# Performance work log

Measured on AMD Instinct MI355X. Metric: run time of the kernel, lower is better.

Reference implementation:

```python
import jax, jax.numpy as jnp
import numpy as np

NUM_HEADS = 12


def setup_inputs() -> dict:
    key = jax.random.key(0)
    k0, k1, k2 = jax.random.split(key, 3)
    B, S, D = 2, 2048, 1536
    scale = 1.0 / np.sqrt(D)
    return {
        "hidden_states": jax.random.normal(k0, (B, S, D), dtype=jnp.float32),
        "W_fc": jax.random.normal(k1, (D, D), dtype=jnp.float32) * scale,
        "b_fc": jnp.zeros((D,), dtype=jnp.float32),
        "W_proj": jax.random.normal(k2, (D, D), dtype=jnp.float32) * scale,
        "b_proj": jnp.zeros((D,), dtype=jnp.float32),
    }


def reference(hidden_states, W_fc, b_fc, W_proj, b_proj):
    B, S, D = hidden_states.shape
    H = NUM_HEADS
    hd = D // H
    # value_states: [B, H, S, hd] (key_states == value_states in the original)
    v = (hidden_states @ W_fc.T + b_fc).reshape(B, S, H, hd).transpose(0, 2, 1, 3)
    # Uniform-weight causal sliding-window attention, window_h = 2^(h+1)-1.
    i = jnp.arange(S)[:, None]          # query pos
    j = jnp.arange(S)[None, :]          # key pos
    w = (2 ** jnp.arange(1, H + 1, dtype=jnp.int32) - 1)[:, None, None]  # [H,1,1]
    mask = (j <= i) & (j >= i - w + 1)                                    # [H,S,S]
    valid_len = jnp.minimum(i + 1, w).astype(v.dtype)                     # [H,S,1]
    attn = jnp.where(mask, 1.0 / valid_len, 0.0)                          # [H,S,S]
    # [H,S,S] x [B,H,S,hd] -> [B,S,H,hd] -> [B,S,D]
    out = jnp.einsum("hqk,bhkd->bqhd", attn, v).reshape(B, S, D)
    attn_weights = jnp.broadcast_to(attn[None], (B, H, S, S))
    return out @ W_proj.T + b_proj, attn_weights
```

## Files before the change

### kernel.cpp

```cpp
#include <hip/hip_runtime.h>
#include <hip/hip_bf16.h>

#define S_LEN   2048
#define DMODEL  1536
#define NBATCH  2
#define NHEADS  12
#define MROWS   (NBATCH * S_LEN)
#define NCHUNK  64

#define NGEMM_BLK  384

#define AW_TOT4   25165824u
#define AW_CVT4    2097152u
#define AW_G1_4    9437184u
#define AW_WA4     4718592u
#define AW_G2_4    8912896u

#define CVT_BLK    10752
#define CVT_AWBLK  1024
#define AW_BLK     3072
#define WA_BLK     3072
#define WA_AWBLK   2048

typedef unsigned short u16;
typedef __attribute__((ext_vector_type(8))) short bf16x8;
typedef __attribute__((ext_vector_type(4))) float f32x4;

__device__ __forceinline__ u16 f2bf(float x) {
  unsigned u = __float_as_uint(x);
  u += 0x7fffu + ((u >> 16) & 1u);
  return (u16)(u >> 16);
}
__device__ __forceinline__ float bf2f(u16 x) {
  return __uint_as_float(((unsigned)x) << 16);
}

__device__ __forceinline__ void aw_stream(f32x4* __restrict__ aw, unsigned aw0,
                                          unsigned awcnt, unsigned blk, unsigned nblk) {
  const unsigned stride = nblk * 256u;
  const unsigned end = aw0 + awcnt;
  for (unsigned t = aw0 + blk * 256u + threadIdx.x; t < end; t += stride) {
    int j0 = (int)(t & 511u) << 2;
    int i  = (int)(t >> 9) & (S_LEN - 1);
    int bh = (int)(t >> 20);
    int h  = bh >= NHEADS ? bh - NHEADS : bh;
    int w  = (2 << h) - 1;
    float inv = 1.0f / (float)min(i + 1, w);
    int lo = i - w + 1;
    f32x4 r;
    r.x = (j0     <= i && j0     >= lo) ? inv : 0.f;
    r.y = (j0 + 1 <= i && j0 + 1 >= lo) ? inv : 0.f;
    r.z = (j0 + 2 <= i && j0 + 2 >= lo) ? inv : 0.f;
    r.w = (j0 + 3 <= i && j0 + 3 >= lo) ? inv : 0.f;
    aw[t] = r;
  }
}

#define N4_HID  1572864
#define N4_W    589824
__global__ void cvt_all(const float4* __restrict__ h, const float4* __restrict__ wf,
                        const float4* __restrict__ wp, ushort4* __restrict__ ho,
                        ushort4* __restrict__ wfo, ushort4* __restrict__ wpo,
                        f32x4* __restrict__ aw, unsigned aw0, unsigned awcnt) {
  if ((int)blockIdx.x >= CVT_BLK) {
    aw_stream(aw, aw0, awcnt, blockIdx.x - CVT_BLK, CVT_AWBLK);
    return;
  }
  int t = blockIdx.x * blockDim.x + threadIdx.x;
  const float4* src;
  ushort4* dst;
  int idx;
  if (t < N4_HID)            { src = h;  dst = ho;  idx = t; }
  else if (t < N4_HID + N4_W){ src = wf; dst = wfo; idx = t - N4_HID; }
  else                       { src = wp; dst = wpo; idx = t - N4_HID - N4_W; }
  float4 f = src[idx];
  ushort4 o;
  o.x = f2bf(f.x); o.y = f2bf(f.y); o.z = f2bf(f.z); o.w = f2bf(f.w);
  dst[idx] = o;
}

__device__ __forceinline__ void gld_lds16(u16* lds, const u16* g) {
  __builtin_amdgcn_global_load_lds(
      (const __attribute__((address_space(1))) unsigned int*)g,
      (__attribute__((address_space(3))) unsigned int*)lds, 16, 0, 0);
}

template <bool WITH_CSUM, typename CT>
__global__ __launch_bounds__(256)
void gemm_aw(const u16* __restrict__ A, const u16* __restrict__ B,
             const float* __restrict__ bias, CT* __restrict__ C,
             float* __restrict__ cs, f32x4* __restrict__ aw,
             unsigned aw0, unsigned awcnt, int Ndim, int Kdim) {
  if ((int)blockIdx.x >= NGEMM_BLK) {
    aw_stream(aw, aw0, awcnt, blockIdx.x - NGEMM_BLK, gridDim.x - NGEMM_BLK);
    return;
  }

  __shared__ __align__(16) u16 As[2][128 * 32];
  __shared__ __align__(16) u16 Bs[2][128 * 32];
  __shared__ float colpart[4][128];

  const int tid  = threadIdx.x;
  const int wave = tid >> 6;
  const int lane = tid & 63;
  const int l15  = lane & 15;
  const int quad = lane >> 4;
  const int bm = (blockIdx.x / (DMODEL / 128)) * 128;
  const int bn = (blockIdx.x % (DMODEL / 128)) * 128;
  const int wm = (wave >> 1) * 64;
  const int wn = (wave & 1) * 64;

  f32x4 acc[4][4] = {};

  const int srow = wave * 32 + (lane >> 2);
  const int skk  = (lane & 3) * 8;
  const u16* gA = A + (size_t)(bm + srow) * Kdim + skk;
  const u16* gB = B + (size_t)(bn + srow) * Kdim + skk;
  const int lofs = (wave * 32) * 32;
  const size_t rstep16 = (size_t)16 * Kdim;

  gld_lds16(&As[0][lofs],           gA);
  gld_lds16(&As[0][lofs + 16 * 32], gA + rstep16);
  gld_lds16(&Bs[0][lofs],           gB);
  gld_lds16(&Bs[0][lofs + 16 * 32], gB + rstep16);

  int cur = 0;
  for (int k0 = 0; k0 < Kdim; k0 += 32) {
    __syncthreads();
    if (k0 + 32 < Kdim) {
      const int nxt = cur ^ 1;
      gld_lds16(&As[nxt][lofs],           gA + k0 + 32);
      gld_lds16(&As[nxt][lofs + 16 * 32], gA + k0 + 32 + rstep16);
      gld_lds16(&Bs[nxt][lofs],           gB + k0 + 32);
      gld_lds16(&Bs[nxt][lofs + 16 * 32], gB + k0 + 32 + rstep16);
    }

    bf16x8 af[4], bfr[4];
#pragma unroll
    for (int i = 0; i < 4; ++i)
      af[i] = *(const bf16x8*)&As[cur][(wm + i * 16 + l15) * 32 + quad * 8];
#pragma unroll
    for (int j = 0; j < 4; ++j)
      bfr[j] = *(const bf16x8*)&Bs[cur][(wn + j * 16 + l15) * 32 + quad * 8];
#pragma unroll
    for (int i = 0; i < 4; ++i)
#pragma unroll
      for (int j = 0; j < 4; ++j)
        acc[i][j] = __builtin_amdgcn_mfma_f32_16x16x32_bf16(af[i], bfr[j], acc[i][j], 0, 0, 0);
    cur ^= 1;
  }

  const int r0 = quad * 4;
#pragma unroll
  for (int j = 0; j < 4; ++j) {
    const int col = bn + wn + j * 16 + l15;
    const float bj = bias[col];
    float sA = 0.f, sB = 0.f;
#pragma unroll
    for (int i = 0; i < 4; ++i) {
      const int row = bm + wm + i * 16 + r0;
#pragma unroll
      for (int r = 0; r < 4; ++r) {
        float cv = acc[i][j][r] + bj;
        if constexpr (sizeof(CT) == 2)
          C[(size_t)(row + r) * Ndim + col] = (CT)f2bf(cv);
        else
          C[(size_t)(row + r) * Ndim + col] = (CT)cv;
        if (WITH_CSUM) { if (i < 2) sA += cv; else sB += cv; }
      }
    }
    if (WITH_CSUM) {
      sA += __shfl_xor(sA, 16); sA += __shfl_xor(sA, 32);
      sB += __shfl_xor(sB, 16); sB += __shfl_xor(sB, 32);
      if (quad == 0) {
        colpart[(wm >> 5) | 0][wn + j * 16 + l15] = sA;
        colpart[(wm >> 5) | 1][wn + j * 16 + l15] = sB;
      }
    }
  }
  if (WITH_CSUM) {
    __syncthreads();
    if (tid < 128) {
      const int b  = bm >> 11;
      const int c0 = (bm & 2047) >> 5;
#pragma unroll
      for (int g = 0; g < 4; ++g)
        cs[((size_t)b * NCHUNK + c0 + g) * DMODEL + bn + tid] = colpart[g][tid];
    }
  }
}

__global__ void winavg_aw(const u16* __restrict__ v, const float* __restrict__ cs,
                          u16* __restrict__ A2,
                          f32x4* __restrict__ aw, unsigned aw0, unsigned awcnt) {
  if ((int)blockIdx.x >= WA_BLK) {
    aw_stream(aw, aw0, awcnt, blockIdx.x - WA_BLK, WA_AWBLK);
    return;
  }
  int t = blockIdx.x * blockDim.x + threadIdx.x;
  int d = t % DMODEL;
  int s = (t / DMODEL) & 255;
  int b = t / (DMODEL * 256);
  const int h = d >> 7;
  const int w = (2 << h) - 1;
  const u16* vb  = v + (size_t)b * S_LEN * DMODEL + d;
  const float* cb = cs + (size_t)b * NCHUNK * DMODEL + d;

  const int i0 = s * 8;
  const int clead = i0 >> 5;

  int jf = 0, ct = 0;
  const bool ht = (i0 + 7 >= w);
  if (ht) { jf = max(i0, w) - w; ct = jf > 0 ? (jf - 1) >> 5 : 0; }

  float lead = 0.f, tb = 0.f;
  for (int cc = 0; cc < clead; ++cc) {
    float x = cb[(size_t)cc * DMODEL];
    lead += x;
    if (cc < ct) tb += x;
  }
  for (int r = clead * 32; r < i0; ++r)
    lead += bf2f(vb[(size_t)r * DMODEL]);

  float trail = 0.f;
  if (ht && jf > 0) {
    trail = tb;
    for (int r = ct * 32; r < jf; ++r)
      trail += bf2f(vb[(size_t)r * DMODEL]);
  }

  u16* out = A2 + ((size_t)(b * S_LEN + i0)) * DMODEL + d;
#pragma unroll
  for (int rr = 0; rr < 8; ++rr) {
    const int i = i0 + rr;
    lead += bf2f(vb[(size_t)i * DMODEL]);
    float o;
    if (i < w) {
      o = lead / (float)(i + 1);
    } else {
      trail += bf2f(vb[(size_t)(i - w) * DMODEL]);
      o = (lead - trail) / (float)w;
    }
    out[(size_t)rr * DMODEL] = f2bf(o);
  }
}

extern "C" void kernel_launch(void* const* d_in, const int* in_sizes, int n_in,
                              void* d_out, int out_size, void* d_ws, size_t ws_size,
                              hipStream_t stream) {
  const float* hidden = (const float*)d_in[0];
  const float* W_fc   = (const float*)d_in[1];
  const float* b_fc   = (const float*)d_in[2];
  const float* W_proj = (const float*)d_in[3];
  const float* b_proj = (const float*)d_in[4];
  float* outp = (float*)d_out;
  f32x4* aw = (f32x4*)(outp + (size_t)MROWS * DMODEL);

  char* ws = (char*)d_ws;
  u16*   A16   = (u16*)(ws);
  u16*   Wfc16 = (u16*)(ws + 12582912);
  u16*   Wpj16 = (u16*)(ws + 17301504);
  u16*   v16   = (u16*)(ws + 22020096);
  float* csums = (float*)(ws + 34603008);

  cvt_all<<<CVT_BLK + CVT_AWBLK, 256, 0, stream>>>(
      (const float4*)hidden, (const float4*)W_fc, (const float4*)W_proj,
      (ushort4*)A16, (ushort4*)Wfc16, (ushort4*)Wpj16,
      aw, 0u, AW_CVT4);

  gemm_aw<true, u16><<<NGEMM_BLK + AW_BLK, 256, 0, stream>>>(
      A16, Wfc16, b_fc, v16, csums, aw, AW_CVT4, AW_G1_4, DMODEL, DMODEL);

  winavg_aw<<<WA_BLK + WA_AWBLK, 256, 0, stream>>>(
      v16, csums, A16, aw, AW_CVT4 + AW_G1_4, AW_WA4);

  gemm_aw<false, float><<<NGEMM_BLK + AW_BLK, 256, 0, stream>>>(
      A16, Wpj16, b_proj, outp, nullptr, aw,
      AW_CVT4 + AW_G1_4 + AW_WA4, AW_G2_4, DMODEL, DMODEL);
}
```

Measured before the change: 553.7 us.

## Halve GEMM M-tile to 64 rows, double block count, add nontemporal stores

Shrinks the GEMM block tile from 128x128 to 64x128 and doubles the number of GEMM blocks, so more workgroups cover the CUs. A and B tiles now share one unified LDS buffer loaded in three 16-row groups per wave. Stores of the attention-weights stream and the fp32 GEMM output become nontemporal to reduce cache pollution. Each block gets less data reuse per K step and does more redundant B loads in total.

```diff
diff --git a/kernel.cpp b/kernel.cpp
--- a/kernel.cpp
+++ b/kernel.cpp
@@ -8,7 +8,7 @@
 #define MROWS   (NBATCH * S_LEN)
 #define NCHUNK  64
 
-#define NGEMM_BLK  384
+#define NGEMM_BLK  768
 
 #define AW_TOT4   25165824u
 #define AW_CVT4    2097152u
@@ -52,7 +52,7 @@
     r.y = (j0 + 1 <= i && j0 + 1 >= lo) ? inv : 0.f;
     r.z = (j0 + 2 <= i && j0 + 2 >= lo) ? inv : 0.f;
     r.w = (j0 + 3 <= i && j0 + 3 >= lo) ? inv : 0.f;
-    aw[t] = r;
+    __builtin_nontemporal_store(r, &aw[t]);
   }
 }
 
@@ -96,54 +96,55 @@
     return;
   }
 
-  __shared__ __align__(16) u16 As[2][128 * 32];
-  __shared__ __align__(16) u16 Bs[2][128 * 32];
-  __shared__ float colpart[4][128];
+  __shared__ __align__(16) u16 Ts[2][192 * 32];
+  __shared__ float colpart[2][128];
 
   const int tid  = threadIdx.x;
   const int wave = tid >> 6;
   const int lane = tid & 63;
   const int l15  = lane & 15;
   const int quad = lane >> 4;
-  const int bm = (blockIdx.x / (DMODEL / 128)) * 128;
+  const int bm = (blockIdx.x / (DMODEL / 128)) * 64;
   const int bn = (blockIdx.x % (DMODEL / 128)) * 128;
-  const int wm = (wave >> 1) * 64;
+  const int wm = (wave >> 1) * 32;
   const int wn = (wave & 1) * 64;
 
-  f32x4 acc[4][4] = {};
-
-  const int srow = wave * 32 + (lane >> 2);
-  const int skk  = (lane & 3) * 8;
-  const u16* gA = A + (size_t)(bm + srow) * Kdim + skk;
-  const u16* gB = B + (size_t)(bn + srow) * Kdim + skk;
-  const int lofs = (wave * 32) * 32;
-  const size_t rstep16 = (size_t)16 * Kdim;
-
-  gld_lds16(&As[0][lofs],           gA);
-  gld_lds16(&As[0][lofs + 16 * 32], gA + rstep16);
-  gld_lds16(&Bs[0][lofs],           gB);
-  gld_lds16(&Bs[0][lofs + 16 * 32], gB + rstep16);
+  f32x4 acc[2][4] = {};
+
+  const int lr  = lane >> 2;
+  const int skk = (lane & 3) * 8;
+  const u16* gsrc[3];
+  int lofs[3];
+#pragma unroll
+  for (int g = 0; g < 3; ++g) {
+    const int rg = wave * 48 + g * 16;
+    lofs[g] = rg * 32;
+    gsrc[g] = (rg < 64)
+        ? (A + (size_t)(bm + rg + lr) * Kdim + skk)
+        : (B + (size_t)(bn + rg - 64 + lr) * Kdim + skk);
+  }
+
+#pragma unroll
+  for (int g = 0; g < 3; ++g) gld_lds16(&Ts[0][lofs[g]], gsrc[g]);
 
   int cur = 0;
   for (int k0 = 0; k0 < Kdim; k0 += 32) {
     __syncthreads();
     if (k0 + 32 < Kdim) {
       const int nxt = cur ^ 1;
-      gld_lds16(&As[nxt][lofs],           gA + k0 + 32);
-      gld_lds16(&As[nxt][lofs + 16 * 32], gA + k0 + 32 + rstep16);
-      gld_lds16(&Bs[nxt][lofs],           gB + k0 + 32);
-      gld_lds16(&Bs[nxt][lofs + 16 * 32], gB + k0 + 32 + rstep16);
-    }
-
-    bf16x8 af[4], bfr[4];
-#pragma unroll
-    for (int i = 0; i < 4; ++i)
-      af[i] = *(const bf16x8*)&As[cur][(wm + i * 16 + l15) * 32 + quad * 8];
+#pragma unroll
+      for (int g = 0; g < 3; ++g) gld_lds16(&Ts[nxt][lofs[g]], gsrc[g] + k0 + 32);
+    }
+
+    bf16x8 af[2], bfr[4];
+#pragma unroll
+    for (int i = 0; i < 2; ++i)
+      af[i] = *(const bf16x8*)&Ts[cur][(wm + i * 16 + l15) * 32 + quad * 8];
 #pragma unroll
     for (int j = 0; j < 4; ++j)
-      bfr[j] = *(const bf16x8*)&Bs[cur][(wn + j * 16 + l15) * 32 + quad * 8];
-#pragma unroll
-    for (int i = 0; i < 4; ++i)
+      bfr[j] = *(const bf16x8*)&Ts[cur][(64 + wn + j * 16 + l15) * 32 + quad * 8];
+#pragma unroll
+    for (int i = 0; i < 2; ++i)
 #pragma unroll
       for (int j = 0; j < 4; ++j)
         acc[i][j] = __builtin_amdgcn_mfma_f32_16x16x32_bf16(af[i], bfr[j], acc[i][j], 0, 0, 0);
@@ -155,27 +156,24 @@
   for (int j = 0; j < 4; ++j) {
     const int col = bn + wn + j * 16 + l15;
     const float bj = bias[col];
-    float sA = 0.f, sB = 0.f;
-#pragma unroll
-    for (int i = 0; i < 4; ++i) {
+    float s = 0.f;
+#pragma unroll
+    for (int i = 0; i < 2; ++i) {
       const int row = bm + wm + i * 16 + r0;
 #pragma unroll
       for (int r = 0; r < 4; ++r) {
         float cv = acc[i][j][r] + bj;
-        if constexpr (sizeof(CT) == 2)
+        if constexpr (sizeof(CT) == 2) {
           C[(size_t)(row + r) * Ndim + col] = (CT)f2bf(cv);
-        else
-          C[(size_t)(row + r) * Ndim + col] = (CT)cv;
-        if (WITH_CSUM) { if (i < 2) sA += cv; else sB += cv; }
+        } else {
+          __builtin_nontemporal_store((CT)cv, &C[(size_t)(row + r) * Ndim + col]);
+        }
+        if (WITH_CSUM) s += cv;
       }
     }
     if (WITH_CSUM) {
-      sA += __shfl_xor(sA, 16); sA += __shfl_xor(sA, 32);
-      sB += __shfl_xor(sB, 16); sB += __shfl_xor(sB, 32);
-      if (quad == 0) {
-        colpart[(wm >> 5) | 0][wn + j * 16 + l15] = sA;
-        colpart[(wm >> 5) | 1][wn + j * 16 + l15] = sB;
-      }
+      s += __shfl_xor(s, 16); s += __shfl_xor(s, 32);
+      if (quad == 0) colpart[wm >> 5][wn + j * 16 + l15] = s;
     }
   }
   if (WITH_CSUM) {
@@ -184,7 +182,7 @@
       const int b  = bm >> 11;
       const int c0 = (bm & 2047) >> 5;
 #pragma unroll
-      for (int g = 0; g < 4; ++g)
+      for (int g = 0; g < 2; ++g)
         cs[((size_t)b * NCHUNK + c0 + g) * DMODEL + bn + tid] = colpart[g][tid];
     }
   }
```

New measurement: 541.3 us. 1.02x faster.
